# Kernel tuning notes

Hardware: AMD Instinct MI355X
Metric: run time of the kernel (lower is better)

The kernel has to match this reference:

```python
import jax, jax.numpy as jnp
import numpy as np

N_QUBITS = 6
N_LAYERS = 4
N_ACTIONS = 4
PRE_DIM = 64
BATCH = 262144


def _cnot(state, ctrl, tgt):
    # state: (B, 2,...,2); flip target axis on the control=1 slice
    ca, ta = 1 + ctrl, 1 + tgt
    s0 = jnp.take(state, 0, axis=ca)
    s1 = jnp.take(state, 1, axis=ca)
    ta_in = ta if ta < ca else ta - 1
    s1 = jnp.flip(s1, axis=ta_in)
    return jnp.stack([s0, s1], axis=ca)


def _ry_batched(state, angles_q, q):
    # angles_q: (B,) per-sample RY angle on qubit q (AngleEmbedding)
    h = angles_q * 0.5
    c, s = jnp.cos(h), jnp.sin(h)
    R = jnp.stack([jnp.stack([c, -s], -1), jnp.stack([s, c], -1)], -2)  # (B,2,2)
    st = jnp.moveaxis(state, 1 + q, -1)
    st = jnp.einsum('b...i,bji->b...j', st, R)
    return jnp.moveaxis(st, -1, 1 + q)


def _ry_scalar(state, theta, q):
    h = theta * 0.5
    c, s = jnp.cos(h), jnp.sin(h)
    R = jnp.stack([jnp.stack([c, -s]), jnp.stack([s, c])])  # (2,2)
    st = jnp.moveaxis(state, 1 + q, -1)
    st = st @ R.T  # new_j = sum_i R[j,i] amp_i
    return jnp.moveaxis(st, -1, 1 + q)


def _circuit(xp, qw):
    # xp: (B, n_qubits) angles; qw: (n_layers, n_qubits)
    B = xp.shape[0]
    state = jnp.zeros((B,) + (2,) * N_QUBITS, xp.dtype)
    state = state.at[(slice(None),) + (0,) * N_QUBITS].set(1.0)
    for q in range(N_QUBITS):
        state = _ry_batched(state, xp[:, q], q)
    for l in range(N_LAYERS):
        for i in range(N_QUBITS):
            state = _cnot(state, i, (i + 1) % N_QUBITS)
        for i in range(N_QUBITS):
            state = _ry_scalar(state, qw[l, i], i)
    probs = state * state  # RY/CNOT are real; state stays real
    all_axes = tuple(range(1, N_QUBITS + 1))
    zs = []
    for q in range(N_QUBITS):
        p = jnp.sum(probs, axis=tuple(a for a in all_axes if a != 1 + q))  # (B,2)
        zs.append(p[:, 0] - p[:, 1])
    return jnp.stack(zs, -1)  # (B, n_qubits)


def setup_inputs() -> dict:
    key = jax.random.key(0)
    ks = jax.random.split(key, 10)
    x = jax.random.normal(ks[0], (BATCH, N_QUBITS), jnp.float32)
    sc = 1.0 / np.sqrt(N_QUBITS)
    W1 = jax.random.uniform(ks[1], (PRE_DIM, N_QUBITS), jnp.float32, -sc, sc)
    b1 = jax.random.uniform(ks[2], (PRE_DIM,), jnp.float32, -sc, sc)
    sc2 = 1.0 / np.sqrt(PRE_DIM)
    W2 = jax.random.uniform(ks[3], (N_QUBITS, PRE_DIM), jnp.float32, -sc2, sc2)
    b2 = jax.random.uniform(ks[4], (N_QUBITS,), jnp.float32, -sc2, sc2)
    qw = jax.random.uniform(ks[5], (N_LAYERS, N_QUBITS), jnp.float32, 0.0, 2.0 * np.pi)
    Wp = jax.random.uniform(ks[6], (N_ACTIONS, N_QUBITS), jnp.float32, -sc, sc)
    bp = jax.random.uniform(ks[7], (N_ACTIONS,), jnp.float32, -sc, sc)
    Wv = jax.random.uniform(ks[8], (1, N_QUBITS), jnp.float32, -sc, sc)
    bv = jax.random.uniform(ks[9], (1,), jnp.float32, -sc, sc)
    return {"x": x, "W1": W1, "b1": b1, "W2": W2, "b2": b2, "qw": qw,
            "Wp": Wp, "bp": bp, "Wv": Wv, "bv": bv}


def reference(x, W1, b1, W2, b2, qw, Wp, bp, Wv, bv):
    h = jax.nn.relu(x @ W1.T + b1)
    xp = jax.nn.relu(h @ W2.T + b2)          # (B, n_qubits)
    qout = _circuit(xp, qw)                   # (B, n_qubits)
    policy = jax.nn.softmax(qout @ Wp.T + bp, axis=-1)
    value = (qout @ Wv.T + bv)[:, 0]
    return policy, value
```

## Files before the change

kernel.cpp:

```cpp
#include <hip/hip_runtime.h>
#include <math.h>


#define NQ 6
#define NL 4
#define NA 4
#define PD 64

typedef float v2 __attribute__((ext_vector_type(2)));

__device__ __forceinline__ v2 mk2(float a, float b) { v2 r; r.x = a; r.y = b; return r; }
__device__ __forceinline__ v2 pkfma(v2 a, v2 b, v2 c) { return __builtin_elementwise_fma(a, b, c); }

__global__ __launch_bounds__(256) void qpolicy_kernel(
    const float* __restrict__ x,
    const float* __restrict__ W1,
    const float* __restrict__ b1,
    const float* __restrict__ W2,
    const float* __restrict__ b2,
    const float* __restrict__ qw,
    const float* __restrict__ Wp,
    const float* __restrict__ bp,
    const float* __restrict__ Wv,
    const float* __restrict__ bv,
    float* __restrict__ out,
    int B)
{
    const int tid = blockIdx.x * blockDim.x + threadIdx.x;

    const v2* xv = reinterpret_cast<const v2*>(x + (size_t)tid * NQ);
    const v2 x01 = xv[0], x23 = xv[1], x45 = xv[2];

    const v2* W1v = reinterpret_cast<const v2*>(W1);
    const v2* W2v = reinterpret_cast<const v2*>(W2);

    v2 h2[PD / 2];
#pragma unroll
    for (int j2 = 0; j2 < PD / 2; ++j2) {
        float hj[2];
#pragma unroll
        for (int u = 0; u < 2; ++u) {
            const int j = 2 * j2 + u;
            v2 acc = mk2(b1[j], 0.0f);
            acc = pkfma(x01, W1v[j * 3 + 0], acc);
            acc = pkfma(x23, W1v[j * 3 + 1], acc);
            acc = pkfma(x45, W1v[j * 3 + 2], acc);
            hj[u] = fmaxf(acc.x + acc.y, 0.0f);
        }
        h2[j2] = mk2(hj[0], hj[1]);
    }

    float xp[NQ];
#pragma unroll
    for (int i = 0; i < NQ; ++i) {
        v2 acc = mk2(b2[i], 0.0f);
#pragma unroll
        for (int k = 0; k < PD / 2; ++k) acc = pkfma(h2[k], W2v[i * (PD / 2) + k], acc);
        xp[i] = fmaxf(acc.x + acc.y, 0.0f);
    }

    float cq[NQ], sq[NQ];
#pragma unroll
    for (int q = 0; q < NQ; ++q) __sincosf(0.5f * xp[q], &sq[q], &cq[q]);

    float pr[32];
    pr[0] = 1.0f;
#pragma unroll
    for (int q = 0; q < 5; ++q) {
        const int sz = 1 << q;
#pragma unroll
        for (int k = sz - 1; k >= 0; --k) {
            const float v = pr[k];
            pr[2 * k]     = v * cq[q];
            pr[2 * k + 1] = v * sq[q];
        }
    }
    v2 st[32];
    const v2 cs5 = mk2(cq[5], sq[5]);
#pragma unroll
    for (int k = 0; k < 32; ++k) st[k] = mk2(pr[k], pr[k]) * cs5;

#pragma unroll
    for (int l = 0; l < NL; ++l) {
#pragma unroll
        for (int i = 0; i < 4; ++i) {
            const int mc = 1 << (4 - i), mt = 1 << (3 - i);
#pragma unroll
            for (int k = 0; k < 32; ++k) {
                if ((k & mc) && !(k & mt)) {
                    v2 tmp = st[k]; st[k] = st[k | mt]; st[k | mt] = tmp;
                }
            }
        }
#pragma unroll
        for (int k = 0; k < 32; ++k) {
            if (k & 1) st[k] = __builtin_shufflevector(st[k], st[k], 1, 0);
        }
#pragma unroll
        for (int k = 0; k < 16; ++k) {
            const float tmp = st[k].y; st[k].y = st[k | 16].y; st[k | 16].y = tmp;
        }

        float tv[NQ], sv[NQ];
#pragma unroll
        for (int i = 0; i < NQ; ++i) {
            float hh = 0.5f * qw[l * NQ + i];
            hh = (hh > 1.5707963f) ? (hh - 3.14159265358979f) : hh;
            float sh, ch;
            __sincosf(hh, &sh, &ch);
            sv[i] = sh;
            tv[i] = sh * __builtin_amdgcn_rcpf(1.0f + ch);
        }

#pragma unroll
        for (int i = 0; i < 5; ++i) {
            const int m = 1 << (4 - i);
            const v2 vnt = mk2(-tv[i], -tv[i]);
            const v2 vs  = mk2(sv[i], sv[i]);
#pragma unroll
            for (int k = 0; k < 32; ++k) {
                if (!(k & m)) {
                    v2 a = st[k], b = st[k | m];
                    a = pkfma(vnt, b, a);
                    b = pkfma(vs, a, b);
                    a = pkfma(vnt, b, a);
                    st[k] = a; st[k | m] = b;
                }
            }
        }
        {
            const float nt = -tv[5], s5 = sv[5];
#pragma unroll
            for (int k = 0; k < 32; ++k) {
                float a0 = st[k].x, a1 = st[k].y;
                a0 = fmaf(nt, a1, a0);
                a1 = fmaf(s5, a0, a1);
                a0 = fmaf(nt, a1, a0);
                st[k] = mk2(a0, a1);
            }
        }
    }

    float a[32];
    float S5 = 0.0f;
#pragma unroll
    for (int k = 0; k < 32; ++k) {
        const v2 p = st[k] * st[k];
        a[k] = p.x + p.y;
        S5 += p.x;
    }
    float S0 = 0.0f;
#pragma unroll
    for (int k = 0; k < 16; ++k) S0 += a[k];
    float b16[16];
#pragma unroll
    for (int k = 0; k < 16; ++k) b16[k] = a[k] + a[k | 16];
    float S1 = 0.0f;
#pragma unroll
    for (int k = 0; k < 8; ++k) S1 += b16[k];
    float b8[8];
#pragma unroll
    for (int k = 0; k < 8; ++k) b8[k] = b16[k] + b16[k | 8];
    const float S2 = b8[0] + b8[1] + b8[2] + b8[3];
    float b4[4];
#pragma unroll
    for (int k = 0; k < 4; ++k) b4[k] = b8[k] + b8[k | 4];
    const float S3 = b4[0] + b4[1];
    float b2a[2];
    b2a[0] = b4[0] + b4[2];
    b2a[1] = b4[1] + b4[3];
    const float S4 = b2a[0];
    const float T = b2a[0] + b2a[1];

    float z[NQ];
    z[0] = fmaf(2.0f, S0, -T);
    z[1] = fmaf(2.0f, S1, -T);
    z[2] = fmaf(2.0f, S2, -T);
    z[3] = fmaf(2.0f, S3, -T);
    z[4] = fmaf(2.0f, S4, -T);
    z[5] = fmaf(2.0f, S5, -T);

    float logits[NA];
#pragma unroll
    for (int aidx = 0; aidx < NA; ++aidx) {
        float acc = bp[aidx];
#pragma unroll
        for (int q = 0; q < NQ; ++q) acc = fmaf(z[q], Wp[aidx * NQ + q], acc);
        logits[aidx] = acc;
    }
    float m = logits[0];
#pragma unroll
    for (int aidx = 1; aidx < NA; ++aidx) m = fmaxf(m, logits[aidx]);
    float e[NA];
    float esum = 0.0f;
#pragma unroll
    for (int aidx = 0; aidx < NA; ++aidx) { e[aidx] = __expf(logits[aidx] - m); esum += e[aidx]; }
    const float inv = 1.0f / esum;

    float4 pol;
    pol.x = e[0] * inv; pol.y = e[1] * inv; pol.z = e[2] * inv; pol.w = e[3] * inv;
    reinterpret_cast<float4*>(out)[tid] = pol;

    float v = bv[0];
#pragma unroll
    for (int q = 0; q < NQ; ++q) v = fmaf(z[q], Wv[q], v);
    out[(size_t)B * NA + tid] = v;
}

extern "C" void kernel_launch(void* const* d_in, const int* in_sizes, int n_in,
                              void* d_out, int out_size, void* d_ws, size_t ws_size,
                              hipStream_t stream) {
    const float* x  = (const float*)d_in[0];
    const float* W1 = (const float*)d_in[1];
    const float* b1 = (const float*)d_in[2];
    const float* W2 = (const float*)d_in[3];
    const float* b2 = (const float*)d_in[4];
    const float* qw = (const float*)d_in[5];
    const float* Wp = (const float*)d_in[6];
    const float* bp = (const float*)d_in[7];
    const float* Wv = (const float*)d_in[8];
    const float* bv = (const float*)d_in[9];
    float* out = (float*)d_out;

    const int B = in_sizes[0] / NQ;
    dim3 block(256);
    dim3 grid((B + 255) / 256);
    hipLaunchKernelGGL(qpolicy_kernel, grid, block, 0, stream,
                       x, W1, b1, W2, b2, qw, Wp, bp, Wv, bv, out, B);
}
```

Baseline: 99.22 us.

## Split each sample's quantum state across two lanes using DPP exchanges

Each sample now runs on a pair of adjacent lanes. Each lane holds half of the 64-amplitude state (qubit 0 is split across the two lanes), and the CNOT on qubit 0 and the qubit-0 rotation exchange amplitudes through DPP quad-permute moves. The MLP is refactored to accumulate the second layer on the fly instead of storing all 64 hidden values, and launch bounds now ask for 8 blocks per SM. The aim is to halve register pressure and raise occupancy. In exchange, both lanes repeat the full MLP and sincos work, twice as many threads are launched, and extra cross-lane moves are added.

```diff
diff --git a/kernel.cpp b/kernel.cpp
--- a/kernel.cpp
+++ b/kernel.cpp
@@ -12,7 +12,13 @@
 __device__ __forceinline__ v2 mk2(float a, float b) { v2 r; r.x = a; r.y = b; return r; }
 __device__ __forceinline__ v2 pkfma(v2 a, v2 b, v2 c) { return __builtin_elementwise_fma(a, b, c); }
 
-__global__ __launch_bounds__(256) void qpolicy_kernel(
+__device__ __forceinline__ float dppx1(float v) {
+    int i = __builtin_bit_cast(int, v);
+    i = __builtin_amdgcn_mov_dpp(i, 0xB1, 0xF, 0xF, true);
+    return __builtin_bit_cast(float, i);
+}
+
+__global__ __launch_bounds__(256, 8) void qpolicy_kernel(
     const float* __restrict__ x,
     const float* __restrict__ W1,
     const float* __restrict__ b1,
@@ -26,48 +32,50 @@
     float* __restrict__ out,
     int B)
 {
-    const int tid = blockIdx.x * blockDim.x + threadIdx.x;
-
-    const v2* xv = reinterpret_cast<const v2*>(x + (size_t)tid * NQ);
+    const int t = blockIdx.x * blockDim.x + threadIdx.x;
+    const int s = t >> 1;
+    const bool podd = (t & 1) != 0;
+
+    const v2* xv = reinterpret_cast<const v2*>(x + (size_t)s * NQ);
     const v2 x01 = xv[0], x23 = xv[1], x45 = xv[2];
 
     const v2* W1v = reinterpret_cast<const v2*>(W1);
     const v2* W2v = reinterpret_cast<const v2*>(W2);
 
-    v2 h2[PD / 2];
-#pragma unroll
-    for (int j2 = 0; j2 < PD / 2; ++j2) {
-        float hj[2];
+    v2 xpa[NQ];
+#pragma unroll
+    for (int i = 0; i < NQ; ++i) xpa[i] = mk2(b2[i], 0.0f);
+#pragma unroll
+    for (int k2 = 0; k2 < PD / 2; ++k2) {
+        float hu[2];
 #pragma unroll
         for (int u = 0; u < 2; ++u) {
-            const int j = 2 * j2 + u;
+            const int j = 2 * k2 + u;
             v2 acc = mk2(b1[j], 0.0f);
             acc = pkfma(x01, W1v[j * 3 + 0], acc);
             acc = pkfma(x23, W1v[j * 3 + 1], acc);
             acc = pkfma(x45, W1v[j * 3 + 2], acc);
-            hj[u] = fmaxf(acc.x + acc.y, 0.0f);
-        }
-        h2[j2] = mk2(hj[0], hj[1]);
-    }
-
+            hu[u] = fmaxf(acc.x + acc.y, 0.0f);
+        }
+        const v2 hv = mk2(hu[0], hu[1]);
+#pragma unroll
+        for (int i = 0; i < NQ; ++i)
+            xpa[i] = pkfma(hv, W2v[i * (PD / 2) + k2], xpa[i]);
+    }
     float xp[NQ];
 #pragma unroll
-    for (int i = 0; i < NQ; ++i) {
-        v2 acc = mk2(b2[i], 0.0f);
-#pragma unroll
-        for (int k = 0; k < PD / 2; ++k) acc = pkfma(h2[k], W2v[i * (PD / 2) + k], acc);
-        xp[i] = fmaxf(acc.x + acc.y, 0.0f);
-    }
+    for (int i = 0; i < NQ; ++i) xp[i] = fmaxf(xpa[i].x + xpa[i].y, 0.0f);
 
     float cq[NQ], sq[NQ];
 #pragma unroll
     for (int q = 0; q < NQ; ++q) __sincosf(0.5f * xp[q], &sq[q], &cq[q]);
 
-    float pr[32];
-    pr[0] = 1.0f;
-#pragma unroll
-    for (int q = 0; q < 5; ++q) {
-        const int sz = 1 << q;
+    const float g0 = podd ? sq[0] : cq[0];
+    float pr[16];
+    pr[0] = g0;
+#pragma unroll
+    for (int q = 1; q <= 4; ++q) {
+        const int sz = 1 << (q - 1);
 #pragma unroll
         for (int k = sz - 1; k >= 0; --k) {
             const float v = pr[k];
@@ -75,35 +83,40 @@
             pr[2 * k + 1] = v * sq[q];
         }
     }
-    v2 st[32];
+    v2 st[16];
     const v2 cs5 = mk2(cq[5], sq[5]);
 #pragma unroll
-    for (int k = 0; k < 32; ++k) st[k] = mk2(pr[k], pr[k]) * cs5;
+    for (int j = 0; j < 16; ++j) st[j] = mk2(pr[j], pr[j]) * cs5;
 
 #pragma unroll
     for (int l = 0; l < NL; ++l) {
 #pragma unroll
-        for (int i = 0; i < 4; ++i) {
-            const int mc = 1 << (4 - i), mt = 1 << (3 - i);
-#pragma unroll
-            for (int k = 0; k < 32; ++k) {
-                if ((k & mc) && !(k & mt)) {
-                    v2 tmp = st[k]; st[k] = st[k | mt]; st[k | mt] = tmp;
-                }
-            }
-        }
-#pragma unroll
-        for (int k = 0; k < 32; ++k) {
-            if (k & 1) st[k] = __builtin_shufflevector(st[k], st[k], 1, 0);
-        }
-#pragma unroll
-        for (int k = 0; k < 16; ++k) {
-            const float tmp = st[k].y; st[k].y = st[k | 16].y; st[k | 16].y = tmp;
-        }
-
+        for (int j = 0; j < 8; ++j) {
+            const v2 a = st[j], b = st[j | 8];
+            st[j]     = podd ? b : a;
+            st[j | 8] = podd ? a : b;
+        }
+#pragma unroll
+        for (int j = 0; j < 16; ++j)
+            if ((j & 8) && !(j & 4)) { v2 tmp = st[j]; st[j] = st[j | 4]; st[j | 4] = tmp; }
+#pragma unroll
+        for (int j = 0; j < 16; ++j)
+            if ((j & 4) && !(j & 2)) { v2 tmp = st[j]; st[j] = st[j | 2]; st[j | 2] = tmp; }
+#pragma unroll
+        for (int j = 0; j < 16; ++j)
+            if ((j & 2) && !(j & 1)) { v2 tmp = st[j]; st[j] = st[j | 1]; st[j | 1] = tmp; }
+#pragma unroll
+        for (int j = 0; j < 16; ++j)
+            if (j & 1) st[j] = __builtin_shufflevector(st[j], st[j], 1, 0);
+#pragma unroll
+        for (int j = 0; j < 16; ++j) st[j].y = dppx1(st[j].y);
+
+        float s0r, c0r;
+        __sincosf(0.5f * qw[l * NQ + 0], &s0r, &c0r);
+        const float ssg = podd ? s0r : -s0r;
         float tv[NQ], sv[NQ];
 #pragma unroll
-        for (int i = 0; i < NQ; ++i) {
+        for (int i = 1; i < NQ; ++i) {
             float hh = 0.5f * qw[l * NQ + i];
             hh = (hh > 1.5707963f) ? (hh - 3.14159265358979f) : hh;
             float sh, ch;
@@ -112,65 +125,78 @@
             tv[i] = sh * __builtin_amdgcn_rcpf(1.0f + ch);
         }
 
-#pragma unroll
-        for (int i = 0; i < 5; ++i) {
+        {
+            const v2 c2 = mk2(c0r, c0r), sg2 = mk2(ssg, ssg);
+#pragma unroll
+            for (int j = 0; j < 16; ++j) {
+                v2 o;
+                o.x = dppx1(st[j].x);
+                o.y = dppx1(st[j].y);
+                st[j] = pkfma(sg2, o, st[j] * c2);
+            }
+        }
+#pragma unroll
+        for (int i = 1; i <= 4; ++i) {
             const int m = 1 << (4 - i);
             const v2 vnt = mk2(-tv[i], -tv[i]);
             const v2 vs  = mk2(sv[i], sv[i]);
 #pragma unroll
-            for (int k = 0; k < 32; ++k) {
-                if (!(k & m)) {
-                    v2 a = st[k], b = st[k | m];
+            for (int j = 0; j < 16; ++j) {
+                if (!(j & m)) {
+                    v2 a = st[j], b = st[j | m];
                     a = pkfma(vnt, b, a);
                     b = pkfma(vs, a, b);
                     a = pkfma(vnt, b, a);
-                    st[k] = a; st[k | m] = b;
+                    st[j] = a; st[j | m] = b;
                 }
             }
         }
         {
             const float nt = -tv[5], s5 = sv[5];
 #pragma unroll
-            for (int k = 0; k < 32; ++k) {
-                float a0 = st[k].x, a1 = st[k].y;
+            for (int j = 0; j < 16; ++j) {
+                float a0 = st[j].x, a1 = st[j].y;
                 a0 = fmaf(nt, a1, a0);
                 a1 = fmaf(s5, a0, a1);
                 a0 = fmaf(nt, a1, a0);
-                st[k] = mk2(a0, a1);
+                st[j] = mk2(a0, a1);
             }
         }
     }
 
-    float a[32];
-    float S5 = 0.0f;
-#pragma unroll
-    for (int k = 0; k < 32; ++k) {
-        const v2 p = st[k] * st[k];
-        a[k] = p.x + p.y;
-        S5 += p.x;
-    }
-    float S0 = 0.0f;
-#pragma unroll
-    for (int k = 0; k < 16; ++k) S0 += a[k];
-    float b16[16];
-#pragma unroll
-    for (int k = 0; k < 16; ++k) b16[k] = a[k] + a[k | 16];
-    float S1 = 0.0f;
-#pragma unroll
-    for (int k = 0; k < 8; ++k) S1 += b16[k];
+    float a[16];
+    float S5l = 0.0f;
+#pragma unroll
+    for (int j = 0; j < 16; ++j) {
+        const v2 pp = st[j] * st[j];
+        a[j] = pp.x + pp.y;
+        S5l += pp.x;
+    }
+    float S1l = 0.0f;
+#pragma unroll
+    for (int j = 0; j < 8; ++j) S1l += a[j];
     float b8[8];
 #pragma unroll
-    for (int k = 0; k < 8; ++k) b8[k] = b16[k] + b16[k | 8];
-    const float S2 = b8[0] + b8[1] + b8[2] + b8[3];
+    for (int j = 0; j < 8; ++j) b8[j] = a[j] + a[j | 8];
+    const float S2l = b8[0] + b8[1] + b8[2] + b8[3];
     float b4[4];
 #pragma unroll
-    for (int k = 0; k < 4; ++k) b4[k] = b8[k] + b8[k | 4];
-    const float S3 = b4[0] + b4[1];
-    float b2a[2];
-    b2a[0] = b4[0] + b4[2];
-    b2a[1] = b4[1] + b4[3];
-    const float S4 = b2a[0];
-    const float T = b2a[0] + b2a[1];
+    for (int j = 0; j < 4; ++j) b4[j] = b8[j] + b8[j | 4];
+    const float S3l = b4[0] + b4[1];
+    float b2v[2];
+    b2v[0] = b4[0] + b4[2];
+    b2v[1] = b4[1] + b4[3];
+    const float S4l = b2v[0];
+    const float Tl  = b2v[0] + b2v[1];
+
+    const float To = dppx1(Tl);
+    const float T  = Tl + To;
+    const float S0 = podd ? To : Tl;
+    const float S1 = S1l + dppx1(S1l);
+    const float S2 = S2l + dppx1(S2l);
+    const float S3 = S3l + dppx1(S3l);
+    const float S4 = S4l + dppx1(S4l);
+    const float S5 = S5l + dppx1(S5l);
 
     float z[NQ];
     z[0] = fmaf(2.0f, S0, -T);
@@ -199,12 +225,15 @@
 
     float4 pol;
     pol.x = e[0] * inv; pol.y = e[1] * inv; pol.z = e[2] * inv; pol.w = e[3] * inv;
-    reinterpret_cast<float4*>(out)[tid] = pol;
 
     float v = bv[0];
 #pragma unroll
     for (int q = 0; q < NQ; ++q) v = fmaf(z[q], Wv[q], v);
-    out[(size_t)B * NA + tid] = v;
+
+    if (!podd) {
+        reinterpret_cast<float4*>(out)[s] = pol;
+        out[(size_t)B * NA + s] = v;
+    }
 }
 
 extern "C" void kernel_launch(void* const* d_in, const int* in_sizes, int n_in,
@@ -224,7 +253,7 @@
 
     const int B = in_sizes[0] / NQ;
     dim3 block(256);
-    dim3 grid((B + 255) / 256);
+    dim3 grid((2 * B + 255) / 256);
     hipLaunchKernelGGL(qpolicy_kernel, grid, block, 0, stream,
                        x, W1, b1, W2, b2, qw, Wp, bp, Wv, bv, out, B);
 }
```

Result: slower. 136.9 us (+37.9%).
